# Performance work log

Hardware: AMD Instinct MI355X
Metric: run time of the kernel (lower is better)

## Reference

```python
import jax, jax.numpy as jnp
import numpy as np

V = 100000   # vocab (input_size == output_size)
H = 300      # glove_embed_dim == hidden_size
L = 64       # max_length
B = 64       # batch_size


def gru_step(x, h, W_ih, W_hh, b_ih, b_hh):
    # PyTorch nn.GRU single step. x,h: [B,H]; W_*: [3H,H]; b_*: [3H]
    gi = x @ W_ih.T + b_ih
    gh = h @ W_hh.T + b_hh
    i_r, i_z, i_n = jnp.split(gi, 3, axis=-1)
    h_r, h_z, h_n = jnp.split(gh, 3, axis=-1)
    r = jax.nn.sigmoid(i_r + h_r)
    z = jax.nn.sigmoid(i_z + h_z)
    n = jnp.tanh(i_n + r * h_n)
    return (1.0 - z) * n + z * h


def setup_inputs() -> dict:
    key = jax.random.key(0)
    ks = jax.random.split(key, 12)
    s = 1.0 / np.sqrt(H)
    u = lambda k, shape: jax.random.uniform(k, shape, jnp.float32, -s, s)
    return {
        "input": jax.random.randint(ks[0], (L, B), 0, V),
        "emb": jax.random.normal(ks[1], (V, H), jnp.float32),
        "enc_W_ih": u(ks[2], (3 * H, H)), "enc_W_hh": u(ks[3], (3 * H, H)),
        "enc_b_ih": u(ks[4], (3 * H,)), "enc_b_hh": u(ks[5], (3 * H,)),
        "dec_W_ih": u(ks[6], (3 * H, H)), "dec_W_hh": u(ks[7], (3 * H, H)),
        "dec_b_ih": u(ks[8], (3 * H,)), "dec_b_hh": u(ks[9], (3 * H,)),
        "out_W": u(ks[10], (V, H)), "out_b": u(ks[11], (V,)),
    }


def reference(input, emb, enc_W_ih, enc_W_hh, enc_b_ih, enc_b_hh,
              dec_W_ih, dec_W_hh, dec_b_ih, dec_b_hh, out_W, out_b):
    max_len, batch = input.shape

    # ---- encoder: GRU over token embeddings ----
    def enc_step(h, ids):
        x = emb[ids]  # [B,H]
        h_new = gru_step(x, h, enc_W_ih, enc_W_hh, enc_b_ih, enc_b_hh)
        return h_new, None

    h0 = jnp.zeros((batch, H), jnp.float32)
    enc_h, _ = jax.lax.scan(enc_step, h0, input)

    # ---- decoder: greedy generation for max_len steps ----
    def dec_step(carry, _):
        h, ids = carry
        x = jax.nn.relu(emb[ids])
        h_new = gru_step(x, h, dec_W_ih, dec_W_hh, dec_b_ih, dec_b_hh)
        logp = jax.nn.log_softmax(h_new @ out_W.T + out_b, axis=1)  # [B,V]
        new_ids = jnp.argmax(logp, axis=1)  # topk(1)
        return (h_new, new_ids), new_ids.astype(jnp.float32)

    init_ids = jnp.zeros((batch,), jnp.int64 if input.dtype == jnp.int64 else jnp.int32)
    _, out = jax.lax.scan(dec_step, (enc_h, init_ids), None, length=max_len)
    return out  # [max_len, batch] float token ids
```

## Files before the change

kernel.cpp:

```cpp
#include <hip/hip_runtime.h>

#define HD 300
#define KC 75
#define BD 64
#define VD 100000
#define LD 64
#define NM32 3126
#define NT16 6252
#define MARGIN 0.05f

typedef unsigned long long u64;
typedef short short8 __attribute__((ext_vector_type(8)));
typedef float f32x4 __attribute__((ext_vector_type(4)));

__device__ __forceinline__ float sigm(float x) { return 1.0f / (1.0f + expf(-x)); }

__device__ __forceinline__ int tidx(int k, int b) {
  return (k >> 2) * 256 + b * 4 + (k & 3);
}

__device__ __forceinline__ unsigned enc32(float f) {
  unsigned u = __float_as_uint(f);
  return (u & 0x80000000u) ? ~u : (u | 0x80000000u);
}
__device__ __forceinline__ float dec32(unsigned e) {
  unsigned u = (e & 0x80000000u) ? (e & 0x7FFFFFFFu) : ~e;
  return __uint_as_float(u);
}
__device__ __forceinline__ unsigned short f2bf(float f) {
  unsigned u = __float_as_uint(f);
  unsigned r = u + 0x7FFFu + ((u >> 16) & 1u);
  return (unsigned short)(r >> 16);
}
__device__ __forceinline__ u64 shfl64(u64 v, int m) {
  int lo = __shfl_xor((int)(unsigned)v, m, 64);
  int hi = __shfl_xor((int)(unsigned)(v >> 32), m, 64);
  return ((u64)(unsigned)hi << 32) | (unsigned)lo;
}
__device__ __forceinline__ void top2(u64 k, u64& b, u64& r) {
  if (k > b) { r = b; b = k; } else if (k > r) r = k;
}

__global__ __launch_bounds__(320) void k_prep(
    const int* __restrict__ input, const float* __restrict__ emb,
    float* __restrict__ xall)
{
  const int t = blockIdx.x, b = blockIdx.y;
  const int k = threadIdx.x;
  if (k >= HD) return;
  const int id = input[t * BD + b];
  xall[t * (KC * 256) + tidx(k, b)] = emb[(size_t)id * HD + k];
}

__global__ __launch_bounds__(320) void k_init(
    float* __restrict__ hT, const float* __restrict__ emb, float* __restrict__ xdec)
{
  const int b = blockIdx.x;
  const int k = threadIdx.x;
  if (k >= HD) return;
  hT[tidx(k, b)] = 0.f;
  xdec[tidx(k, b)] = fmaxf(emb[k], 0.f);
}

__global__ __launch_bounds__(384) void k_gru(
    const float* __restrict__ xT, const float* __restrict__ hT_in,
    const float* __restrict__ W_ih, const float* __restrict__ W_hh,
    const float* __restrict__ b_ih, const float* __restrict__ b_hh,
    float* __restrict__ hT_out)
{
  const int w = __builtin_amdgcn_readfirstlane(threadIdx.x >> 6);
  const int b = threadIdx.x & 63;
  const int m = w & 1;
  const int g = w >> 1;
  const int i0 = blockIdx.x * 4;

  const float* src = m ? hT_in : xT;
  const float* M   = m ? W_hh : W_ih;
  const float* row0 = M + (size_t)(g * HD + i0) * HD;

  float4 a0 = {0,0,0,0}, a1 = {0,0,0,0}, a2 = {0,0,0,0}, a3 = {0,0,0,0};

  for (int kc = 0; kc < KC; kc++) {
    const float4 s = *(const float4*)(src + kc * 256 + b * 4);
    const float4 w0 = *(const float4*)(row0 + kc * 4);
    const float4 w1 = *(const float4*)(row0 + HD + kc * 4);
    const float4 w2 = *(const float4*)(row0 + 2 * HD + kc * 4);
    const float4 w3 = *(const float4*)(row0 + 3 * HD + kc * 4);
    a0.x += w0.x * s.x; a0.y += w0.y * s.y; a0.z += w0.z * s.z; a0.w += w0.w * s.w;
    a1.x += w1.x * s.x; a1.y += w1.y * s.y; a1.z += w1.z * s.z; a1.w += w1.w * s.w;
    a2.x += w2.x * s.x; a2.y += w2.y * s.y; a2.z += w2.z * s.z; a2.w += w2.w * s.w;
    a3.x += w3.x * s.x; a3.y += w3.y * s.y; a3.z += w3.z * s.z; a3.w += w3.w * s.w;
  }

  const float* bias = m ? b_hh : b_ih;
  __shared__ float sg[2][3][4][64];
  sg[m][g][0][b] = (a0.x + a0.y) + (a0.z + a0.w) + bias[g * HD + i0 + 0];
  sg[m][g][1][b] = (a1.x + a1.y) + (a1.z + a1.w) + bias[g * HD + i0 + 1];
  sg[m][g][2][b] = (a2.x + a2.y) + (a2.z + a2.w) + bias[g * HD + i0 + 2];
  sg[m][g][3][b] = (a3.x + a3.y) + (a3.z + a3.w) + bias[g * HD + i0 + 3];
  __syncthreads();

  if (w < 4) {
    const int r = w;
    const int i = i0 + r;
    const float rr = sigm(sg[0][0][r][b] + sg[1][0][r][b]);
    const float zz = sigm(sg[0][1][r][b] + sg[1][1][r][b]);
    const float nn = tanhf(sg[0][2][r][b] + rr * sg[1][2][r][b]);
    const float hp = hT_in[tidx(i, b)];
    hT_out[tidx(i, b)] = (1.f - zz) * nn + zz * hp;
  }
}

__global__ __launch_bounds__(256) void k_pack(
    const float* __restrict__ outW, unsigned* __restrict__ Wp)
{
  const int t16 = blockIdx.x;
  const int d = threadIdx.x;
  const int lane = d >> 2, p = d & 3;
  const int v = t16 * 16 + (lane & 15);
  for (int kt = 0; kt < 10; kt++) {
    const int k = kt * 32 + (lane >> 4) * 8 + 2 * p;
    float f0 = 0.f, f1 = 0.f;
    if (v < VD) {
      if (k < HD)     f0 = outW[(size_t)v * HD + k];
      if (k + 1 < HD) f1 = outW[(size_t)v * HD + k + 1];
    }
    const unsigned out = (unsigned)f2bf(f0) | ((unsigned)f2bf(f1) << 16);
    Wp[((size_t)t16 * 10 + kt) * 256 + d] = out;
  }
}

__global__ __launch_bounds__(256) void k_packh(
    const float* __restrict__ hT, unsigned* __restrict__ hbp)
{
  const int i = blockIdx.x * 256 + threadIdx.x;
  if (i >= 10240) return;
  const int p = i & 3, lane = (i >> 2) & 63, nt = (i >> 8) & 3, kt = i >> 10;
  const int b = nt * 16 + (lane & 15);
  const int k = kt * 32 + (lane >> 4) * 8 + 2 * p;
  float f0 = (k < HD)     ? hT[tidx(k, b)]     : 0.f;
  float f1 = (k + 1 < HD) ? hT[tidx(k + 1, b)] : 0.f;
  hbp[i] = (unsigned)f2bf(f0) | ((unsigned)f2bf(f1) << 16);
}

template <bool PACKED>
__global__ __launch_bounds__(256) void k_projbf(
    const unsigned* __restrict__ Wp, const float* __restrict__ outW,
    const unsigned* __restrict__ hbp, const float* __restrict__ outb,
    u64* __restrict__ bbuf)
{
  __shared__ unsigned hlds[10240];
  for (int i = threadIdx.x; i < 10240; i += 256) hlds[i] = hbp[i];
  __syncthreads();

  const int w = __builtin_amdgcn_readfirstlane(threadIdx.x >> 6);
  const int lane = threadIdx.x & 63;
  const int m32 = blockIdx.x * 4 + w;
  if (m32 >= NM32) return;
  const int m0 = m32 * 32;
  const int quad = lane >> 4;

  f32x4 acc[2][4];
#pragma unroll
  for (int mt = 0; mt < 2; mt++)
#pragma unroll
    for (int nt = 0; nt < 4; nt++) acc[mt][nt] = f32x4{0.f, 0.f, 0.f, 0.f};

  const int t0 = m32 * 2;

  for (int kt = 0; kt < 10; kt++) {
    short8 a[2];
    if (PACKED) {
#pragma unroll
      for (int mt = 0; mt < 2; mt++)
        a[mt] = *(const short8*)(Wp + ((size_t)(t0 + mt) * 10 + kt) * 256 + lane * 4);
    } else {
#pragma unroll
      for (int mt = 0; mt < 2; mt++) {
        const int v = (t0 + mt) * 16 + (lane & 15);
        const int kb = kt * 32 + quad * 8;
        const int vc = (v < VD) ? v : (VD - 1);
        short8 tmp;
#pragma unroll
        for (int e = 0; e < 8; e++) {
          const int kk = kb + e;
          const float f = (kk < HD && v < VD) ? outW[(size_t)vc * HD + kk] : 0.f;
          tmp[e] = (short)f2bf(f);
        }
        a[mt] = tmp;
      }
    }
#pragma unroll
    for (int nt = 0; nt < 4; nt++) {
      const short8 bf = *(const short8*)(&hlds[((kt * 4 + nt) << 8) + lane * 4]);
#pragma unroll
      for (int mt = 0; mt < 2; mt++)
        acc[mt][nt] = __builtin_amdgcn_mfma_f32_16x16x32_bf16(a[mt], bf, acc[mt][nt], 0, 0, 0);
    }
  }

  u64 best[4], run[4];
#pragma unroll
  for (int nt = 0; nt < 4; nt++) { best[nt] = 0ull; run[nt] = 0ull; }

#pragma unroll
  for (int mt = 0; mt < 2; mt++) {
    const int vb = m0 + mt * 16 + quad * 4;
    const int vbc = (vb <= VD - 4) ? vb : (VD - 4);
    const float4 ob = *(const float4*)(outb + vbc);
#pragma unroll
    for (int nt = 0; nt < 4; nt++) {
#pragma unroll
      for (int reg = 0; reg < 4; reg++) {
        const int v = vb + reg;
        if (v < VD) {
          const float obv = (reg == 0) ? ob.x : (reg == 1) ? ob.y : (reg == 2) ? ob.z : ob.w;
          const float val = acc[mt][nt][reg] + obv;
          const u64 key = ((u64)enc32(val) << 32) | (u64)(0xFFFFFFFFu - (unsigned)v);
          top2(key, best[nt], run[nt]);
        }
      }
    }
  }

#pragma unroll
  for (int nt = 0; nt < 4; nt++) {
    u64 ob = shfl64(best[nt], 16), orr = shfl64(run[nt], 16);
    top2(ob, best[nt], run[nt]); top2(orr, best[nt], run[nt]);
    ob = shfl64(best[nt], 32); orr = shfl64(run[nt], 32);
    top2(ob, best[nt], run[nt]); top2(orr, best[nt], run[nt]);
  }

  u64 wb = best[0], wr = run[0];
  if (quad == 1) { wb = best[1]; wr = run[1]; }
  if (quad == 2) { wb = best[2]; wr = run[2]; }
  if (quad == 3) { wb = best[3]; wr = run[3]; }
  u64* dst = bbuf + (size_t)lane * (NM32 * 2) + (size_t)m32 * 2;
  dst[0] = wb; dst[1] = wr;
}

__global__ __launch_bounds__(256) void k_fin2(
    const u64* __restrict__ bbuf, const float* __restrict__ hT,
    const float* __restrict__ outW, const float* __restrict__ outb,
    const float* __restrict__ emb,
    float* __restrict__ out_row, float* __restrict__ xdec)
{
  const int b = blockIdx.x;
  const int tid = threadIdx.x;
  const u64* keys = bbuf + (size_t)b * (NM32 * 2);

  __shared__ u64 red[256];
  u64 local = 0ull;
  for (int i = tid; i < NM32 * 2; i += 256) local = max(local, keys[i]);
  red[tid] = local;
  __syncthreads();
  for (int s2 = 128; s2 > 0; s2 >>= 1) {
    if (tid < s2) red[tid] = max(red[tid], red[tid + s2]);
    __syncthreads();
  }

  __shared__ unsigned s_te;
  __shared__ int s_n;
  if (tid == 0) {
    const float mv = dec32((unsigned)(red[0] >> 32));
    s_te = enc32(mv - MARGIN);
    s_n = 0;
  }
  __syncthreads();
  const unsigned te = s_te;

  __shared__ int cand[256];
  for (int i = tid; i < NM32 * 2; i += 256) {
    const u64 k = keys[i];
    if ((unsigned)(k >> 32) >= te && k != 0ull) {
      const int slot = atomicAdd(&s_n, 1);
      if (slot < 256) cand[slot] = (int)(0xFFFFFFFFu - (unsigned)k);
    }
  }
  __syncthreads();
  const int n = min(s_n, 256);

  u64 bk = 0ull;
  if (tid < n) {
    const int v = cand[tid];
    const float* wr = outW + (size_t)v * HD;
    float acc = 0.f;
    for (int k = 0; k < HD; k++) acc += wr[k] * hT[tidx(k, b)];
    acc += outb[v];
    bk = ((u64)enc32(acc) << 32) | (u64)(0xFFFFFFFFu - (unsigned)v);
  }
  red[tid] = bk;
  __syncthreads();
  for (int s2 = 128; s2 > 0; s2 >>= 1) {
    if (tid < s2) red[tid] = max(red[tid], red[tid + s2]);
    __syncthreads();
  }

  __shared__ int s_id;
  if (tid == 0) {
    const int id = (int)(0xFFFFFFFFu - (unsigned)(red[0] & 0xFFFFFFFFull));
    out_row[b] = (float)id;
    s_id = id;
  }
  __syncthreads();

  const int id = s_id;
  for (int k = tid; k < HD; k += 256)
    xdec[tidx(k, b)] = fmaxf(emb[(size_t)id * HD + k], 0.f);
}

extern "C" void kernel_launch(void* const* d_in, const int* in_sizes, int n_in,
                              void* d_out, int out_size, void* d_ws, size_t ws_size,
                              hipStream_t stream) {
  const int*   input  = (const int*)d_in[0];
  const float* emb    = (const float*)d_in[1];
  const float* eWih   = (const float*)d_in[2];
  const float* eWhh   = (const float*)d_in[3];
  const float* eBih   = (const float*)d_in[4];
  const float* eBhh   = (const float*)d_in[5];
  const float* dWih   = (const float*)d_in[6];
  const float* dWhh   = (const float*)d_in[7];
  const float* dBih   = (const float*)d_in[8];
  const float* dBhh   = (const float*)d_in[9];
  const float* outW   = (const float*)d_in[10];
  const float* outb   = (const float*)d_in[11];
  float* out = (float*)d_out;

  const size_t wpBytes = (size_t)NT16 * 10 * 1024;
  size_t need = wpBytes + 3201024 + 40960 + 5145600 + 6 * 256;
  const bool packed = ws_size >= need;

  size_t off = 0;
  auto take = [&](size_t nbytes) -> char* {
    char* p = (char*)d_ws + off;
    off += (nbytes + 255) & ~(size_t)255;
    return p;
  };

  unsigned* Wp = packed ? (unsigned*)take(wpBytes) : nullptr;
  u64*      bbuf = (u64*)take((size_t)BD * NM32 * 2 * 8);
  unsigned* hbp  = (unsigned*)take(40960);
  float* hA   = (float*)take(76800);
  float* hB   = (float*)take(76800);
  float* xdec = (float*)take(76800);
  float* xall = (float*)take((size_t)LD * 76800);

  if (packed) k_pack<<<NT16, 256, 0, stream>>>(outW, Wp);
  k_prep<<<dim3(LD, BD), 320, 0, stream>>>(input, emb, xall);
  k_init<<<BD, 320, 0, stream>>>(hA, emb, xdec);

  for (int t = 0; t < LD; t++) {
    float* hin  = (t & 1) ? hB : hA;
    float* hout = (t & 1) ? hA : hB;
    k_gru<<<75, 384, 0, stream>>>(xall + t * (KC * 256), hin,
                                  eWih, eWhh, eBih, eBhh, hout);
  }

  for (int s = 0; s < LD; s++) {
    float* hin  = (s & 1) ? hB : hA;
    float* hout = (s & 1) ? hA : hB;
    k_gru<<<75, 384, 0, stream>>>(xdec, hin, dWih, dWhh, dBih, dBhh, hout);
    k_packh<<<40, 256, 0, stream>>>(hout, hbp);
    if (packed)
      k_projbf<true><<<782, 256, 0, stream>>>(Wp, outW, hbp, outb, bbuf);
    else
      k_projbf<false><<<782, 256, 0, stream>>>(Wp, outW, hbp, outb, bbuf);
    k_fin2<<<BD, 256, 0, stream>>>(bbuf, hout, outW, outb, emb, out + s * BD, xdec);
  }
}
```

Measured before the change: 6.827 ms.

## Fuse h packing into GRU, split-K GRU, prefetch projection loads, shuffle reductions

The GRU kernel now splits the K loop across two halves of a 768-thread block and, in decode steps, writes the bf16 MFMA-packed hidden state directly, which removes the separate k_packh launch. The projection kernel issues its first W fragment load before the LDS fill, double-buffers A loads across k-steps and copies h with 16-byte vectors. The final argmax kernel replaces its LDS tree reductions with wave shuffles and vectorises the candidate rescoring dot product. Risks are extra LDS and register pressure in the larger GRU block, and the zero-init of hbp padding now lives in k_init.

```diff
diff --git a/kernel.cpp b/kernel.cpp
--- a/kernel.cpp
+++ b/kernel.cpp
@@ -37,6 +37,7 @@
   int hi = __shfl_xor((int)(unsigned)(v >> 32), m, 64);
   return ((u64)(unsigned)hi << 32) | (unsigned)lo;
 }
+__device__ __forceinline__ u64 umax64(u64 a, u64 b) { return a > b ? a : b; }
 __device__ __forceinline__ void top2(u64 k, u64& b, u64& r) {
   if (k > b) { r = b; b = k; } else if (k > r) r = k;
 }
@@ -53,25 +54,31 @@
 }
 
 __global__ __launch_bounds__(320) void k_init(
-    float* __restrict__ hT, const float* __restrict__ emb, float* __restrict__ xdec)
+    float* __restrict__ hT, const float* __restrict__ emb, float* __restrict__ xdec,
+    unsigned* __restrict__ hbp)
 {
   const int b = blockIdx.x;
   const int k = threadIdx.x;
+  const int gi = b * 320 + k;
+  if (gi < 10240) hbp[gi] = 0u;
   if (k >= HD) return;
   hT[tidx(k, b)] = 0.f;
   xdec[tidx(k, b)] = fmaxf(emb[k], 0.f);
 }
 
-__global__ __launch_bounds__(384) void k_gru(
+template <bool PACK>
+__global__ __launch_bounds__(768) void k_gru(
     const float* __restrict__ xT, const float* __restrict__ hT_in,
     const float* __restrict__ W_ih, const float* __restrict__ W_hh,
     const float* __restrict__ b_ih, const float* __restrict__ b_hh,
-    float* __restrict__ hT_out)
+    float* __restrict__ hT_out, unsigned* __restrict__ hbp)
 {
   const int w = __builtin_amdgcn_readfirstlane(threadIdx.x >> 6);
   const int b = threadIdx.x & 63;
-  const int m = w & 1;
-  const int g = w >> 1;
+  const int half = (w >= 6) ? 1 : 0;
+  const int ww = w - 6 * half;
+  const int m = ww & 1;
+  const int g = ww >> 1;
   const int i0 = blockIdx.x * 4;
 
   const float* src = m ? hT_in : xT;
@@ -80,7 +87,9 @@
 
   float4 a0 = {0,0,0,0}, a1 = {0,0,0,0}, a2 = {0,0,0,0}, a3 = {0,0,0,0};
 
-  for (int kc = 0; kc < KC; kc++) {
+  const int kcB = half ? 38 : 0;
+  const int kcE = half ? KC : 38;
+  for (int kc = kcB; kc < kcE; kc++) {
     const float4 s = *(const float4*)(src + kc * 256 + b * 4);
     const float4 w0 = *(const float4*)(row0 + kc * 4);
     const float4 w1 = *(const float4*)(row0 + HD + kc * 4);
@@ -93,21 +102,50 @@
   }
 
   const float* bias = m ? b_hh : b_ih;
-  __shared__ float sg[2][3][4][64];
-  sg[m][g][0][b] = (a0.x + a0.y) + (a0.z + a0.w) + bias[g * HD + i0 + 0];
-  sg[m][g][1][b] = (a1.x + a1.y) + (a1.z + a1.w) + bias[g * HD + i0 + 1];
-  sg[m][g][2][b] = (a2.x + a2.y) + (a2.z + a2.w) + bias[g * HD + i0 + 2];
-  sg[m][g][3][b] = (a3.x + a3.y) + (a3.z + a3.w) + bias[g * HD + i0 + 3];
+  __shared__ float sg[2][2][3][4][64];
+  const float bb0 = half ? 0.f : bias[g * HD + i0 + 0];
+  const float bb1 = half ? 0.f : bias[g * HD + i0 + 1];
+  const float bb2 = half ? 0.f : bias[g * HD + i0 + 2];
+  const float bb3 = half ? 0.f : bias[g * HD + i0 + 3];
+  sg[half][m][g][0][b] = (a0.x + a0.y) + (a0.z + a0.w) + bb0;
+  sg[half][m][g][1][b] = (a1.x + a1.y) + (a1.z + a1.w) + bb1;
+  sg[half][m][g][2][b] = (a2.x + a2.y) + (a2.z + a2.w) + bb2;
+  sg[half][m][g][3][b] = (a3.x + a3.y) + (a3.z + a3.w) + bb3;
+
+  __shared__ float hsh[4][64];
   __syncthreads();
 
   if (w < 4) {
     const int r = w;
     const int i = i0 + r;
-    const float rr = sigm(sg[0][0][r][b] + sg[1][0][r][b]);
-    const float zz = sigm(sg[0][1][r][b] + sg[1][1][r][b]);
-    const float nn = tanhf(sg[0][2][r][b] + rr * sg[1][2][r][b]);
+    const float xr = sg[0][0][0][r][b] + sg[1][0][0][r][b];
+    const float hr = sg[0][1][0][r][b] + sg[1][1][0][r][b];
+    const float xz = sg[0][0][1][r][b] + sg[1][0][1][r][b];
+    const float hz = sg[0][1][1][r][b] + sg[1][1][1][r][b];
+    const float xn = sg[0][0][2][r][b] + sg[1][0][2][r][b];
+    const float hn = sg[0][1][2][r][b] + sg[1][1][2][r][b];
+    const float rr = sigm(xr + hr);
+    const float zz = sigm(xz + hz);
+    const float nn = tanhf(xn + rr * hn);
     const float hp = hT_in[tidx(i, b)];
-    hT_out[tidx(i, b)] = (1.f - zz) * nn + zz * hp;
+    const float h  = (1.f - zz) * nn + zz * hp;
+    hT_out[tidx(i, b)] = h;
+    if (PACK) hsh[r][b] = h;
+  }
+
+  if (PACK) {
+    __syncthreads();
+    if (w < 2) {
+      const int k = i0 + 2 * w;
+      const unsigned outp =
+          (unsigned)f2bf(hsh[2 * w][b]) | ((unsigned)f2bf(hsh[2 * w + 1][b]) << 16);
+      const int kt = k >> 5;
+      const int q  = (k >> 3) & 3;
+      const int p  = (k >> 1) & 3;
+      const int nt = b >> 4;
+      const int ln = q * 16 + (b & 15);
+      hbp[((kt * 4 + nt) << 8) + ln * 4 + p] = outp;
+    }
   }
 }
 
@@ -130,34 +168,19 @@
   }
 }
 
-__global__ __launch_bounds__(256) void k_packh(
-    const float* __restrict__ hT, unsigned* __restrict__ hbp)
-{
-  const int i = blockIdx.x * 256 + threadIdx.x;
-  if (i >= 10240) return;
-  const int p = i & 3, lane = (i >> 2) & 63, nt = (i >> 8) & 3, kt = i >> 10;
-  const int b = nt * 16 + (lane & 15);
-  const int k = kt * 32 + (lane >> 4) * 8 + 2 * p;
-  float f0 = (k < HD)     ? hT[tidx(k, b)]     : 0.f;
-  float f1 = (k + 1 < HD) ? hT[tidx(k + 1, b)] : 0.f;
-  hbp[i] = (unsigned)f2bf(f0) | ((unsigned)f2bf(f1) << 16);
-}
-
 template <bool PACKED>
 __global__ __launch_bounds__(256) void k_projbf(
     const unsigned* __restrict__ Wp, const float* __restrict__ outW,
     const unsigned* __restrict__ hbp, const float* __restrict__ outb,
     u64* __restrict__ bbuf)
 {
-  __shared__ unsigned hlds[10240];
-  for (int i = threadIdx.x; i < 10240; i += 256) hlds[i] = hbp[i];
-  __syncthreads();
+  __shared__ __align__(16) unsigned hlds[10240];
 
   const int w = __builtin_amdgcn_readfirstlane(threadIdx.x >> 6);
   const int lane = threadIdx.x & 63;
   const int m32 = blockIdx.x * 4 + w;
-  if (m32 >= NM32) return;
-  const int m0 = m32 * 32;
+  const int m32c = (m32 < NM32) ? m32 : (NM32 - 1);
+  const int t0 = m32c * 2;
   const int quad = lane >> 4;
 
   f32x4 acc[2][4];
@@ -166,14 +189,11 @@
 #pragma unroll
     for (int nt = 0; nt < 4; nt++) acc[mt][nt] = f32x4{0.f, 0.f, 0.f, 0.f};
 
-  const int t0 = m32 * 2;
-
-  for (int kt = 0; kt < 10; kt++) {
-    short8 a[2];
+  auto LOADA = [&](short8* dst, int kt) {
     if (PACKED) {
 #pragma unroll
       for (int mt = 0; mt < 2; mt++)
-        a[mt] = *(const short8*)(Wp + ((size_t)(t0 + mt) * 10 + kt) * 256 + lane * 4);
+        dst[mt] = *(const short8*)(Wp + ((size_t)(t0 + mt) * 10 + kt) * 256 + lane * 4);
     } else {
 #pragma unroll
       for (int mt = 0; mt < 2; mt++) {
@@ -187,18 +207,40 @@
           const float f = (kk < HD && v < VD) ? outW[(size_t)vc * HD + kk] : 0.f;
           tmp[e] = (short)f2bf(f);
         }
-        a[mt] = tmp;
+        dst[mt] = tmp;
       }
     }
+  };
+
+  auto COMPUTE = [&](short8* a, int kt) {
 #pragma unroll
     for (int nt = 0; nt < 4; nt++) {
       const short8 bf = *(const short8*)(&hlds[((kt * 4 + nt) << 8) + lane * 4]);
-#pragma unroll
-      for (int mt = 0; mt < 2; mt++)
-        acc[mt][nt] = __builtin_amdgcn_mfma_f32_16x16x32_bf16(a[mt], bf, acc[mt][nt], 0, 0, 0);
-    }
-  }
-
+      acc[0][nt] = __builtin_amdgcn_mfma_f32_16x16x32_bf16(a[0], bf, acc[0][nt], 0, 0, 0);
+      acc[1][nt] = __builtin_amdgcn_mfma_f32_16x16x32_bf16(a[1], bf, acc[1][nt], 0, 0, 0);
+    }
+  };
+
+  short8 aA[2], aB[2];
+  LOADA(aA, 0);
+
+  {
+    const uint4* hb4 = (const uint4*)hbp;
+    uint4* hl4 = (uint4*)hlds;
+    for (int i = threadIdx.x; i < 2560; i += 256) hl4[i] = hb4[i];
+  }
+  __syncthreads();
+  if (m32 >= NM32) return;
+
+#pragma unroll
+  for (int kp = 0; kp < 5; kp++) {
+    LOADA(aB, 2 * kp + 1);
+    COMPUTE(aA, 2 * kp);
+    if (kp < 4) LOADA(aA, 2 * kp + 2);
+    COMPUTE(aB, 2 * kp + 1);
+  }
+
+  const int m0 = m32 * 32;
   u64 best[4], run[4];
 #pragma unroll
   for (int nt = 0; nt < 4; nt++) { best[nt] = 0ull; run[nt] = 0ull; }
@@ -247,22 +289,27 @@
 {
   const int b = blockIdx.x;
   const int tid = threadIdx.x;
+  const int w = tid >> 6, lane = tid & 63;
   const u64* keys = bbuf + (size_t)b * (NM32 * 2);
 
-  __shared__ u64 red[256];
   u64 local = 0ull;
-  for (int i = tid; i < NM32 * 2; i += 256) local = max(local, keys[i]);
-  red[tid] = local;
-  __syncthreads();
-  for (int s2 = 128; s2 > 0; s2 >>= 1) {
-    if (tid < s2) red[tid] = max(red[tid], red[tid + s2]);
-    __syncthreads();
-  }
-
+  {
+    const ulonglong2* k2 = (const ulonglong2*)keys;
+    for (int i = tid; i < NM32; i += 256) {
+      const ulonglong2 v = k2[i];
+      local = umax64(local, umax64(v.x, v.y));
+    }
+  }
+  for (int mm = 1; mm <= 32; mm <<= 1) local = umax64(local, shfl64(local, mm));
+
+  __shared__ u64 wmax[4];
   __shared__ unsigned s_te;
   __shared__ int s_n;
+  if (lane == 0) wmax[w] = local;
+  __syncthreads();
   if (tid == 0) {
-    const float mv = dec32((unsigned)(red[0] >> 32));
+    const u64 mx = umax64(umax64(wmax[0], wmax[1]), umax64(wmax[2], wmax[3]));
+    const float mv = dec32((unsigned)(mx >> 32));
     s_te = enc32(mv - MARGIN);
     s_n = 0;
   }
@@ -283,22 +330,24 @@
   u64 bk = 0ull;
   if (tid < n) {
     const int v = cand[tid];
-    const float* wr = outW + (size_t)v * HD;
+    const float4* wr4 = (const float4*)(outW + (size_t)v * HD);
     float acc = 0.f;
-    for (int k = 0; k < HD; k++) acc += wr[k] * hT[tidx(k, b)];
+    for (int c = 0; c < KC; c++) {
+      const float4 wv = wr4[c];
+      const float4 hv = *(const float4*)(hT + c * 256 + b * 4);
+      acc += wv.x * hv.x + wv.y * hv.y + wv.z * hv.z + wv.w * hv.w;
+    }
     acc += outb[v];
     bk = ((u64)enc32(acc) << 32) | (u64)(0xFFFFFFFFu - (unsigned)v);
   }
-  red[tid] = bk;
-  __syncthreads();
-  for (int s2 = 128; s2 > 0; s2 >>= 1) {
-    if (tid < s2) red[tid] = max(red[tid], red[tid + s2]);
-    __syncthreads();
-  }
+  for (int mm = 1; mm <= 32; mm <<= 1) bk = umax64(bk, shfl64(bk, mm));
+  if (lane == 0) wmax[w] = bk;
+  __syncthreads();
 
   __shared__ int s_id;
   if (tid == 0) {
-    const int id = (int)(0xFFFFFFFFu - (unsigned)(red[0] & 0xFFFFFFFFull));
+    const u64 mx = umax64(umax64(wmax[0], wmax[1]), umax64(wmax[2], wmax[3]));
+    const int id = (int)(0xFFFFFFFFu - (unsigned)(mx & 0xFFFFFFFFull));
     out_row[b] = (float)id;
     s_id = id;
   }
@@ -347,20 +396,19 @@
 
   if (packed) k_pack<<<NT16, 256, 0, stream>>>(outW, Wp);
   k_prep<<<dim3(LD, BD), 320, 0, stream>>>(input, emb, xall);
-  k_init<<<BD, 320, 0, stream>>>(hA, emb, xdec);
+  k_init<<<BD, 320, 0, stream>>>(hA, emb, xdec, hbp);
 
   for (int t = 0; t < LD; t++) {
     float* hin  = (t & 1) ? hB : hA;
     float* hout = (t & 1) ? hA : hB;
-    k_gru<<<75, 384, 0, stream>>>(xall + t * (KC * 256), hin,
-                                  eWih, eWhh, eBih, eBhh, hout);
+    k_gru<false><<<75, 768, 0, stream>>>(xall + t * (KC * 256), hin,
+                                         eWih, eWhh, eBih, eBhh, hout, hbp);
   }
 
   for (int s = 0; s < LD; s++) {
     float* hin  = (s & 1) ? hB : hA;
     float* hout = (s & 1) ? hA : hB;
-    k_gru<<<75, 384, 0, stream>>>(xdec, hin, dWih, dWhh, dBih, dBhh, hout);
-    k_packh<<<40, 256, 0, stream>>>(hout, hbp);
+    k_gru<true><<<75, 768, 0, stream>>>(xdec, hin, dWih, dWhh, dBih, dBhh, hout, hbp);
     if (packed)
       k_projbf<true><<<782, 256, 0, stream>>>(Wp, outW, hbp, outb, bbuf);
     else
```

Result: faster. 6.539 ms (-4.2%).
